# Performance work log

Measured on AMD Instinct MI355X. Metric: run time of the kernel, lower is better.

## Reference

```python
import jax, jax.numpy as jnp
import numpy as np

H = 8          # heads
KP = 6         # num_sparse keypoint tokens per group
NUM_PATCHES = 256


def _build_mask(N, Nk):
    # mask_q: [H, 3, N] bool, query token (g=0, i=0) disabled
    mask_q = np.ones((H, 3, N), dtype=bool)
    mask_q[:, 0, 0] = False
    # mask_k: [H, 3, Nk] bool, key token j=0 disabled for all groups
    mask_k = np.ones((H, 3, Nk), dtype=bool)
    mask_k[:, :, 0] = False
    keep = mask_q[:, :, :, None] & mask_k[:, :, None, :]  # [H,3,N,Nk]
    return jnp.asarray(~keep)  # True where masked out


def setup_inputs() -> dict:
    key = jax.random.key(0)
    k1, k2, k3 = jax.random.split(key, 3)
    B, G, N, D = 64, 3, NUM_PATCHES + KP, 512
    x = jax.random.normal(k1, (B, G, N, D), dtype=jnp.float32)
    w_qkv = jax.random.normal(k2, (D, 3 * D), dtype=jnp.float32) * (D ** -0.5)
    w_out = jax.random.normal(k3, (D, D), dtype=jnp.float32) * (D ** -0.5)
    b_out = jnp.zeros((D,), dtype=jnp.float32)
    return {"x": x, "w_qkv": w_qkv, "w_out": w_out, "b_out": b_out}


def reference(x, w_qkv, w_out, b_out):
    B, G, N, D = x.shape
    Dh = D // H
    scale = D ** -0.5  # scale_with_head=False

    qkv = x @ w_qkv  # [B,G,N,3D]
    q, k, v = jnp.split(qkv, 3, axis=-1)

    def to_heads(t):  # b g n (h d) -> b h g n d
        return t.reshape(B, G, N, H, Dh).transpose(0, 3, 1, 2, 4)

    q, k, v = to_heads(q), to_heads(k), to_heads(v)

    # gather keypoint K/V from all groups, shared across every group
    k_kp = k[:, :, :, :KP].reshape(B, H, 1, G * KP, Dh)
    v_kp = v[:, :, :, :KP].reshape(B, H, 1, G * KP, Dh)
    k_kp = jnp.broadcast_to(k_kp, (B, H, G, G * KP, Dh))
    v_kp = jnp.broadcast_to(v_kp, (B, H, G, G * KP, Dh))
    k = jnp.concatenate([k_kp, k[:, :, :, KP:]], axis=3)  # [B,H,G,Nk,Dh]
    v = jnp.concatenate([v_kp, v[:, :, :, KP:]], axis=3)
    Nk = k.shape[3]

    dots = jnp.einsum('bhgid,bhgjd->bhgij', q, k) * scale
    masked = _build_mask(N, Nk)  # [H,3,N,Nk], broadcasts over B
    neg = -jnp.finfo(dots.dtype).max
    dots = jnp.where(masked[None], neg, dots)

    attn = jax.nn.softmax(dots, axis=-1)
    out = jnp.einsum('bhgij,bhgjd->bhgid', attn, v)
    out = out.transpose(0, 2, 3, 1, 4).reshape(B, G, N, D)  # b h g n d -> b g n (h d)
    out = out @ w_out + b_out
    return out, dots
```

## Files before the change

### kernel.cpp

```cpp
#include <hip/hip_runtime.h>
#include <float.h>
#include <math.h>

#define B_   64
#define G_   3
#define N_   262
#define D_   512
#define H_   8
#define DH   64
#define KP_  6
#define NKP  18
#define NK   274
#define TD3  1536
#define M_   50304
#define SCALE 0.044194173824159216f
#define LOG2E 1.4426950408889634f

typedef unsigned short u16;
typedef __attribute__((ext_vector_type(4))) float f32x4;
typedef __attribute__((ext_vector_type(2))) float f32x2;
typedef float f32x4u __attribute__((ext_vector_type(4), aligned(4)));
typedef __attribute__((ext_vector_type(8))) short bf16x8;

__device__ __forceinline__ u16 f2bf(float f) {
    unsigned int u = __float_as_uint(f);
    u += 0x7FFFu + ((u >> 16) & 1u);
    return (u16)(u >> 16);
}
__device__ __forceinline__ unsigned pack2bf(float lo, float hi) {
    unsigned ul = __float_as_uint(lo); ul += 0x7FFFu + ((ul >> 16) & 1u);
    unsigned uh = __float_as_uint(hi); uh += 0x7FFFu + ((uh >> 16) & 1u);
    return (ul >> 16) | (uh & 0xFFFF0000u);
}
__device__ __forceinline__ float mask_val() { return __uint_as_float(0xFF7F0000u); }

__device__ __forceinline__ void gload16(const void* g, void* l) {
    __builtin_amdgcn_global_load_lds(
        (const __attribute__((address_space(1))) unsigned int*)g,
        (__attribute__((address_space(3))) unsigned int*)l, 16, 0, 0);
}

__global__ __launch_bounds__(256)
void tcast(const float* __restrict__ w, u16* __restrict__ wT, int K, int N)
{
    int idx = blockIdx.x * 256 + threadIdx.x;
    if (idx < K * N) {
        int nn = idx / K, kk = idx - nn * K;
        wT[idx] = f2bf(w[(size_t)kk * N + nn]);
    }
}

template<int AF32, int OUT_BF16>
__global__ __launch_bounds__(512)
void gemm_bf16(const float* __restrict__ Af, const u16* __restrict__ Ab,
               const u16* __restrict__ WT,
               float* __restrict__ Cf, u16* __restrict__ Cb,
               const float* __restrict__ bias, int Ndim, int Kdim)
{
    __shared__ u16 Asm[128 * 64];
    __shared__ u16 Bsm[256 * 64];

    const int tid  = threadIdx.x;
    const int lane = tid & 63;
    const int wid  = tid >> 6;
    const int l15  = lane & 15;
    const int lg   = lane >> 4;
    const int wr   = (wid & 1) * 64;
    const int wc   = (wid >> 1) * 64;
    const int row0 = blockIdx.y * 128;
    const int col0 = blockIdx.x * 256;

    const float* fsrcA[2];
    const u16*   bsrcA[2];
    #pragma unroll
    for (int i = 0; i < 2; ++i) {
        int slot = i * 512 + tid;
        int r = slot >> 3;
        int sblk = (slot & 7) ^ (r & 7);
        if (AF32) fsrcA[i] = Af + (size_t)(row0 + r) * Kdim + sblk * 8;
        else      bsrcA[i] = Ab + (size_t)(row0 + r) * Kdim + sblk * 8;
    }
    const u16* srcB[4];
    #pragma unroll
    for (int i = 0; i < 4; ++i) {
        int slot = i * 512 + tid;
        int r = slot >> 3;
        int sblk = (slot & 7) ^ (r & 7);
        srcB[i] = WT + (size_t)(col0 + r) * Kdim + sblk * 8;
    }

    f32x4 acc[4][4] = {};

    for (int k0 = 0; k0 < Kdim; k0 += 64) {
        #pragma unroll
        for (int i = 0; i < 4; ++i)
            gload16(srcB[i] + k0, &Bsm[(i * 512 + wid * 64) * 8]);
        if (AF32) {
            #pragma unroll
            for (int i = 0; i < 2; ++i) {
                float4 v0 = *(const float4*)(fsrcA[i] + k0);
                float4 v1 = *(const float4*)(fsrcA[i] + k0 + 4);
                u16 t[8] = { f2bf(v0.x), f2bf(v0.y), f2bf(v0.z), f2bf(v0.w),
                             f2bf(v1.x), f2bf(v1.y), f2bf(v1.z), f2bf(v1.w) };
                *(uint4*)&Asm[(i * 512 + tid) * 8] = *(const uint4*)t;
            }
        } else {
            #pragma unroll
            for (int i = 0; i < 2; ++i)
                gload16(bsrcA[i] + k0, &Asm[(i * 512 + wid * 64) * 8]);
        }
        __syncthreads();
        #pragma unroll
        for (int kk = 0; kk < 2; ++kk) {
            const int xb = (kk * 4 + lg) ^ (l15 & 7);
            bf16x8 a[4], b[4];
            #pragma unroll
            for (int m = 0; m < 4; ++m) a[m] = *(const bf16x8*)&Asm[(wr + m * 16 + l15) * 64 + xb * 8];
            #pragma unroll
            for (int n = 0; n < 4; ++n) b[n] = *(const bf16x8*)&Bsm[(wc + n * 16 + l15) * 64 + xb * 8];
            #pragma unroll
            for (int m = 0; m < 4; ++m)
                #pragma unroll
                for (int n = 0; n < 4; ++n)
                    acc[m][n] = __builtin_amdgcn_mfma_f32_16x16x32_bf16(a[m], b[n], acc[m][n], 0, 0, 0);
        }
        __syncthreads();
    }

    const int rbase = row0 + wr + lg * 4;
    const int cbase = col0 + wc + l15;
    #pragma unroll
    for (int m = 0; m < 4; ++m)
        #pragma unroll
        for (int n = 0; n < 4; ++n) {
            const int col = cbase + n * 16;
            #pragma unroll
            for (int r = 0; r < 4; ++r) {
                const int row = rbase + m * 16 + r;
                float v = acc[m][n][r];
                if (OUT_BF16) Cb[(size_t)row * Ndim + col] = f2bf(v);
                else          Cf[(size_t)row * Ndim + col] = v + bias[col];
            }
        }
}

__global__ __launch_bounds__(512, 1)
void attn_bf16(const u16* __restrict__ qkv, float* __restrict__ dots,
               u16* __restrict__ otmp)
{
    __shared__ u16 Ks[288 * 72];
    __shared__ u16 Vt[64 * 296];
    __shared__ float rowbuf[8][8 * 276];

    const int tid  = threadIdx.x;
    const int lane = tid & 63;
    const int wid  = tid >> 6;
    const int l15  = lane & 15;
    const int lg   = lane >> 4;

    const int bhg = blockIdx.x;
    const int b   = bhg / (H_ * G_);
    const int h   = (bhg / G_) % H_;
    const int g   = bhg % G_;
    const int rowbase = (b * G_ + g) * N_;
    const size_t dbase0 = (((size_t)(b * H_ + h) * G_ + g) * N_) * NK;

    for (int it = 0; it < 5; ++it) {
        int lin = tid + it * 512;
        if (lin < 2304) {
            int tok = lin >> 3, kg = (lin & 7) << 3;
            uint4 kv = make_uint4(0, 0, 0, 0), vv = make_uint4(0, 0, 0, 0);
            if (tok < NK) {
                int gs, ns;
                if (tok < NKP) { gs = tok / KP_; ns = tok - gs * KP_; }
                else           { gs = g;         ns = tok - NKP + KP_; }
                const u16* p = qkv + ((size_t)((b * G_ + gs) * N_ + ns)) * TD3 + h * DH + kg;
                kv = *(const uint4*)(p + D_);
                vv = *(const uint4*)(p + 2 * D_);
            }
            *(uint4*)&Ks[tok * 72 + kg] = kv;
            int slot = ((tok >> 5) << 5) | (((tok & 15) >> 2) << 3) | (((tok >> 4) & 1) << 2) | (tok & 3);
            union { uint4 u4; u16 us[8]; } u; u.u4 = vv;
            #pragma unroll
            for (int e = 0; e < 8; ++e) Vt[(kg + e) * 296 + slot] = u.us[e];
        }
    }
    __syncthreads();

    float* rb = rowbuf[wid];

    for (int t = wid; t < 17; t += 8) {
        const int n0 = t * 16;
        int qrow = n0 + l15; if (qrow > N_ - 1) qrow = N_ - 1;
        const u16* qp = qkv + (size_t)(rowbase + qrow) * TD3 + h * DH;
        bf16x8 qa0 = *(const bf16x8*)(qp + lg * 8);
        bf16x8 qa1 = *(const bf16x8*)(qp + 32 + lg * 8);

        f32x4 c[18];
        __builtin_amdgcn_s_setprio(1);
        #pragma unroll
        for (int jt = 0; jt < 18; ++jt) {
            const u16* kr = &Ks[(jt * 16 + l15) * 72];
            bf16x8 kb0 = *(const bf16x8*)(kr + lg * 8);
            bf16x8 kb1 = *(const bf16x8*)(kr + 32 + lg * 8);
            f32x4 z = {};
            z = __builtin_amdgcn_mfma_f32_16x16x32_bf16(kb0, qa0, z, 0, 0, 0);
            c[jt] = __builtin_amdgcn_mfma_f32_16x16x32_bf16(kb1, qa1, z, 0, 0, 0);
        }
        __builtin_amdgcn_s_setprio(0);

        #pragma unroll
        for (int jt = 0; jt < 18; ++jt)
            #pragma unroll
            for (int rr = 0; rr < 4; ++rr) c[jt][rr] *= SCALE;
        c[0][0] = (lg == 0) ? mask_val() : c[0][0];
        if (g == 0 && t == 0) {
            #pragma unroll
            for (int jt = 0; jt < 18; ++jt)
                #pragma unroll
                for (int rr = 0; rr < 4; ++rr)
                    c[jt][rr] = (l15 == 0) ? mask_val() : c[jt][rr];
        }

        const int ph_of_lane = l15 >> 3;
        const int r8 = l15 & 7;
        #pragma unroll
        for (int ph = 0; ph < 2; ++ph) {
            if (ph_of_lane == ph) {
                float* rr_ = &rb[r8 * 276];
                #pragma unroll
                for (int jt = 0; jt < 17; ++jt)
                    *(f32x4*)&rr_[jt * 16 + 4 * lg] = c[jt];
                if (lg == 0) { f32x2 tl = { c[17][0], c[17][1] }; *(f32x2*)&rr_[272] = tl; }
            }
            const int base_row = n0 + 8 * ph;
            const size_t base_f = dbase0 + (size_t)base_row * NK;
            #pragma unroll
            for (int r = 0; r < 8; ++r) {
                if (base_row + r < N_) {
                    const float* rrb = &rb[r * 276];
                    float* gp = &dots[base_f + (size_t)r * NK];
                    #pragma unroll
                    for (int i2 = 0; i2 < 2; ++i2) {
                        int ch = lane + (i2 << 6);
                        if (ch < 68) {
                            f32x4 v = *(const f32x4*)&rrb[ch * 4];
                            *(f32x4u*)&gp[ch * 4] = v;
                        } else if (ch == 68) {
                            f32x2 v2 = *(const f32x2*)&rrb[272];
                            *(f32x2*)&gp[272] = v2;
                        }
                    }
                }
            }
        }

        c[17][2] = -INFINITY; c[17][3] = -INFINITY;
        c[17][0] = (lg == 0) ? c[17][0] : -INFINITY;
        c[17][1] = (lg == 0) ? c[17][1] : -INFINITY;

        float mx = c[0][0];
        #pragma unroll
        for (int jt = 0; jt < 18; ++jt)
            #pragma unroll
            for (int rr = 0; rr < 4; ++rr) mx = fmaxf(mx, c[jt][rr]);
        mx = fmaxf(mx, __shfl_xor(mx, 16, 64));
        mx = fmaxf(mx, __shfl_xor(mx, 32, 64));
        float s = 0.f;
        #pragma unroll
        for (int jt = 0; jt < 18; ++jt)
            #pragma unroll
            for (int rr = 0; rr < 4; ++rr) {
                float p = exp2f((c[jt][rr] - mx) * LOG2E);
                c[jt][rr] = p;
                s += p;
            }
        s += __shfl_xor(s, 16, 64);
        s += __shfl_xor(s, 32, 64);
        const float inv = 1.f / s;

        f32x4 o[4] = {};
        __builtin_amdgcn_s_setprio(1);
        #pragma unroll
        for (int sl = 0; sl < 9; ++sl) {
            union { bf16x8 v; unsigned u[4]; } pa;
            pa.u[0] = pack2bf(c[2 * sl][0],     c[2 * sl][1]);
            pa.u[1] = pack2bf(c[2 * sl][2],     c[2 * sl][3]);
            pa.u[2] = pack2bf(c[2 * sl + 1][0], c[2 * sl + 1][1]);
            pa.u[3] = pack2bf(c[2 * sl + 1][2], c[2 * sl + 1][3]);
            #pragma unroll
            for (int dt = 0; dt < 4; ++dt) {
                bf16x8 vb = *(const bf16x8*)&Vt[(dt * 16 + l15) * 296 + sl * 32 + lg * 8];
                o[dt] = __builtin_amdgcn_mfma_f32_16x16x32_bf16(pa.v, vb, o[dt], 0, 0, 0);
            }
        }
        __builtin_amdgcn_s_setprio(0);

        u16* ob = (u16*)rb;
        #pragma unroll
        for (int dt = 0; dt < 4; ++dt)
            #pragma unroll
            for (int rr = 0; rr < 4; ++rr) {
                const int q = lg * 4 + rr;
                const float iq = __shfl(inv, q, 64);
                ob[q * 64 + dt * 16 + l15] = f2bf(o[dt][rr] * iq);
            }
        {
            const int vrows = min(16, N_ - n0);
            const int nch = vrows * 8;
            #pragma unroll
            for (int i2 = 0; i2 < 2; ++i2) {
                int ch = lane + (i2 << 6);
                if (ch < nch) {
                    int r = ch >> 3, cp = ch & 7;
                    uint4 v = *(const uint4*)&ob[ch * 8];
                    *(uint4*)(otmp + (size_t)(rowbase + n0 + r) * D_ + h * DH + cp * 8) = v;
                }
            }
        }
    }
}

extern "C" void kernel_launch(void* const* d_in, const int* in_sizes, int n_in,
                              void* d_out, int out_size, void* d_ws, size_t ws_size,
                              hipStream_t stream)
{
    const float* x     = (const float*)d_in[0];
    const float* w_qkv = (const float*)d_in[1];
    const float* w_out = (const float*)d_in[2];
    const float* b_out = (const float*)d_in[3];

    float* out  = (float*)d_out;
    float* dots = out + (size_t)M_ * D_;

    u16* wqkvT = (u16*)d_ws;
    u16* woutT = wqkvT + (size_t)TD3 * D_;
    u16* qkvb  = woutT + (size_t)D_ * D_;
    u16* otmpb = qkvb  + (size_t)M_ * TD3;

    tcast<<<(TD3 * D_ + 255) / 256, 256, 0, stream>>>(w_qkv, wqkvT, D_, TD3);
    tcast<<<(D_ * D_ + 255) / 256, 256, 0, stream>>>(w_out, woutT, D_, D_);

    gemm_bf16<1, 1><<<dim3(TD3 / 256, M_ / 128), 512, 0, stream>>>(
        x, nullptr, wqkvT, nullptr, qkvb, nullptr, TD3, D_);

    attn_bf16<<<dim3(B_ * H_ * G_), 512, 0, stream>>>(qkvb, dots, otmpb);

    gemm_bf16<0, 0><<<dim3(D_ / 256, M_ / 128), 512, 0, stream>>>(
        nullptr, otmpb, woutT, out, nullptr, b_out, D_, D_);
}
```

Baseline: 380.5 us.

## Widen attention blocks to 16 waves and XCD-swizzle GEMM tile order

The attention kernel now runs 1024 threads per block, so 16 waves each take one of the 17 query tiles instead of 8 waves looping over two tiles. The per-wave row staging buffer is halved to 4 rows and the dots store runs in four phases to fit shared memory. The GEMMs switch to a 1D grid with an XCD-aware remap of block index to tile, so neighbouring tiles land on the same XCD and can share its L2. The risk is that the 17th query tile now leaves one wave doing a second pass while 15 sit idle, and the larger block may lower occupancy.

```diff
diff --git a/kernel.cpp b/kernel.cpp
--- a/kernel.cpp
+++ b/kernel.cpp
@@ -40,6 +40,12 @@
         (__attribute__((address_space(3))) unsigned int*)l, 16, 0, 0);
 }
 
+__device__ __forceinline__ int xcd_swz(int orig, int nwg) {
+    int q = nwg >> 3, r = nwg & 7;
+    int xcd = orig & 7, lin = orig >> 3;
+    return (xcd < r ? xcd * (q + 1) : r * (q + 1) + (xcd - r) * q) + lin;
+}
+
 __global__ __launch_bounds__(256)
 void tcast(const float* __restrict__ w, u16* __restrict__ wT, int K, int N)
 {
@@ -67,8 +73,11 @@
     const int lg   = lane >> 4;
     const int wr   = (wid & 1) * 64;
     const int wc   = (wid >> 1) * 64;
-    const int row0 = blockIdx.y * 128;
-    const int col0 = blockIdx.x * 256;
+
+    const int GX   = Ndim / 256;
+    const int v    = xcd_swz(blockIdx.x, gridDim.x);
+    const int row0 = (v / GX) * 128;
+    const int col0 = (v % GX) * 256;
 
     const float* fsrcA[2];
     const u16*   bsrcA[2];
@@ -137,20 +146,20 @@
             #pragma unroll
             for (int r = 0; r < 4; ++r) {
                 const int row = rbase + m * 16 + r;
-                float v = acc[m][n][r];
-                if (OUT_BF16) Cb[(size_t)row * Ndim + col] = f2bf(v);
-                else          Cf[(size_t)row * Ndim + col] = v + bias[col];
-            }
-        }
-}
-
-__global__ __launch_bounds__(512, 1)
+                float vv = acc[m][n][r];
+                if (OUT_BF16) Cb[(size_t)row * Ndim + col] = f2bf(vv);
+                else          Cf[(size_t)row * Ndim + col] = vv + bias[col];
+            }
+        }
+}
+
+__global__ __launch_bounds__(1024, 1)
 void attn_bf16(const u16* __restrict__ qkv, float* __restrict__ dots,
                u16* __restrict__ otmp)
 {
     __shared__ u16 Ks[288 * 72];
     __shared__ u16 Vt[64 * 296];
-    __shared__ float rowbuf[8][8 * 276];
+    __shared__ float rowbuf[16][4 * 276];
 
     const int tid  = threadIdx.x;
     const int lane = tid & 63;
@@ -165,8 +174,8 @@
     const int rowbase = (b * G_ + g) * N_;
     const size_t dbase0 = (((size_t)(b * H_ + h) * G_ + g) * N_) * NK;
 
-    for (int it = 0; it < 5; ++it) {
-        int lin = tid + it * 512;
+    for (int it = 0; it < 3; ++it) {
+        int lin = tid + it * 1024;
         if (lin < 2304) {
             int tok = lin >> 3, kg = (lin & 7) << 3;
             uint4 kv = make_uint4(0, 0, 0, 0), vv = make_uint4(0, 0, 0, 0);
@@ -189,7 +198,7 @@
 
     float* rb = rowbuf[wid];
 
-    for (int t = wid; t < 17; t += 8) {
+    for (int t = wid; t < 17; t += 16) {
         const int n0 = t * 16;
         int qrow = n0 + l15; if (qrow > N_ - 1) qrow = N_ - 1;
         const u16* qp = qkv + (size_t)(rowbase + qrow) * TD3 + h * DH;
@@ -222,30 +231,30 @@
                     c[jt][rr] = (l15 == 0) ? mask_val() : c[jt][rr];
         }
 
-        const int ph_of_lane = l15 >> 3;
-        const int r8 = l15 & 7;
-        #pragma unroll
-        for (int ph = 0; ph < 2; ++ph) {
-            if (ph_of_lane == ph) {
-                float* rr_ = &rb[r8 * 276];
+        const int php = l15 >> 2;
+        const int r4  = l15 & 3;
+        #pragma unroll
+        for (int ph = 0; ph < 4; ++ph) {
+            if (php == ph) {
+                float* rr_ = &rb[r4 * 276];
                 #pragma unroll
                 for (int jt = 0; jt < 17; ++jt)
                     *(f32x4*)&rr_[jt * 16 + 4 * lg] = c[jt];
                 if (lg == 0) { f32x2 tl = { c[17][0], c[17][1] }; *(f32x2*)&rr_[272] = tl; }
             }
-            const int base_row = n0 + 8 * ph;
-            const size_t base_f = dbase0 + (size_t)base_row * NK;
-            #pragma unroll
-            for (int r = 0; r < 8; ++r) {
-                if (base_row + r < N_) {
+            const int base_row = n0 + 4 * ph;
+            #pragma unroll
+            for (int r = 0; r < 4; ++r) {
+                const int row = base_row + r;
+                if (row < N_) {
                     const float* rrb = &rb[r * 276];
-                    float* gp = &dots[base_f + (size_t)r * NK];
+                    float* gp = &dots[dbase0 + (size_t)row * NK];
                     #pragma unroll
                     for (int i2 = 0; i2 < 2; ++i2) {
                         int ch = lane + (i2 << 6);
                         if (ch < 68) {
-                            f32x4 v = *(const f32x4*)&rrb[ch * 4];
-                            *(f32x4u*)&gp[ch * 4] = v;
+                            f32x4 vv = *(const f32x4*)&rrb[ch * 4];
+                            *(f32x4u*)&gp[ch * 4] = vv;
                         } else if (ch == 68) {
                             f32x2 v2 = *(const f32x2*)&rrb[272];
                             *(f32x2*)&gp[272] = v2;
@@ -313,8 +322,8 @@
                 int ch = lane + (i2 << 6);
                 if (ch < nch) {
                     int r = ch >> 3, cp = ch & 7;
-                    uint4 v = *(const uint4*)&ob[ch * 8];
-                    *(uint4*)(otmp + (size_t)(rowbase + n0 + r) * D_ + h * DH + cp * 8) = v;
+                    uint4 vv = *(const uint4*)&ob[ch * 8];
+                    *(uint4*)(otmp + (size_t)(rowbase + n0 + r) * D_ + h * DH + cp * 8) = vv;
                 }
             }
         }
@@ -341,11 +350,11 @@
     tcast<<<(TD3 * D_ + 255) / 256, 256, 0, stream>>>(w_qkv, wqkvT, D_, TD3);
     tcast<<<(D_ * D_ + 255) / 256, 256, 0, stream>>>(w_out, woutT, D_, D_);
 
-    gemm_bf16<1, 1><<<dim3(TD3 / 256, M_ / 128), 512, 0, stream>>>(
+    gemm_bf16<1, 1><<<(TD3 / 256) * (M_ / 128), 512, 0, stream>>>(
         x, nullptr, wqkvT, nullptr, qkvb, nullptr, TD3, D_);
 
-    attn_bf16<<<dim3(B_ * H_ * G_), 512, 0, stream>>>(qkvb, dots, otmpb);
-
-    gemm_bf16<0, 0><<<dim3(D_ / 256, M_ / 128), 512, 0, stream>>>(
+    attn_bf16<<<dim3(B_ * H_ * G_), 1024, 0, stream>>>(qkvb, dots, otmpb);
+
+    gemm_bf16<0, 0><<<(D_ / 256) * (M_ / 128), 512, 0, stream>>>(
         nullptr, otmpb, woutT, out, nullptr, b_out, D_, D_);
 }
```

Measured after the change: 412.3 us. +8.4%, slower.
